# Optimization experiments

Hardware: AMD Instinct MI355X
Metric: run time of the kernel (lower is better)

Reference implementation:

```python
import jax, jax.numpy as jnp
import numpy as np

B, T, D = 4, 2048, 2048
H = 16
HO = D // H  # head_out = 128


def setup_inputs() -> dict:
    key = jax.random.key(0)
    ks = jax.random.split(key, 6)
    x = jax.random.normal(ks[0], (B, T, D), dtype=jnp.float32)
    scale = 0.02
    Wq = jax.random.normal(ks[1], (D, D), dtype=jnp.float32) * scale
    Wk = jax.random.normal(ks[2], (D, D), dtype=jnp.float32) * scale
    Wv = jax.random.normal(ks[3], (D, D), dtype=jnp.float32) * scale
    Wp = jax.random.normal(ks[4], (D, D), dtype=jnp.float32) * scale
    bp = jnp.zeros((D,), dtype=jnp.float32)
    return {"x": x, "Wq": Wq, "Wk": Wk, "Wv": Wv, "Wp": Wp, "bp": bp}


def reference(x, Wq, Wk, Wv, Wp, bp):
    b, t, _ = x.shape
    # QKV projections (weights stored [d_in, d_out])
    q = x @ Wq
    k = x @ Wk
    v = x @ Wv
    split = lambda a: a.reshape(b, t, H, HO).transpose(0, 2, 1, 3)  # [b,H,T,ho]
    qh, kh, vh = split(q), split(k), split(v)
    # Feature attention: contract over tokens -> [b,H,ho,ho]
    scores = jnp.einsum('bhtf,bhtg->bhfg', qh, kh) / jnp.sqrt(jnp.float32(HO))
    weights = jax.nn.softmax(scores, axis=-1)  # dropout p=0.0 (identity)
    # feature_alibi: [1/T, 1/(T-1), ..., 1], broadcast over batch/head/feature
    feat_alibi = (1.0 / jnp.arange(t, 0, -1, dtype=jnp.float32)).reshape(1, 1, t, 1)
    vh = vh + feat_alibi
    # (weights @ v^T)^T : ctx[b,h,t,f] = sum_g weights[b,h,f,g] * v[b,h,t,g]
    ctx = jnp.einsum('bhfg,bhtg->bhtf', weights, vh)
    ctx = ctx.transpose(0, 2, 1, 3).reshape(b, t, H * HO)  # [b,T,d_out]
    return ctx @ Wp + bp
```

## Files before the change

kernel.cpp:

```cpp
#include <hip/hip_runtime.h>
#include <hip/hip_bf16.h>


#define Tt 2048
#define Dd 2048
#define Mm 8192

typedef __attribute__((ext_vector_type(4))) float f32x4;
typedef __attribute__((ext_vector_type(8))) short s16x8;
static_assert(sizeof(s16x8) == 16, "frag size");

typedef const __attribute__((address_space(1))) void* gptr_t;
typedef __attribute__((address_space(3))) void* lptr_t;

__device__ __forceinline__ float bf2f(ushort u) {
    union { unsigned int i; float f; } c; c.i = ((unsigned int)u) << 16; return c.f;
}
__device__ __forceinline__ ushort f2bf(float f) {
    union { float f; unsigned int i; } c; c.f = f;
    return (ushort)((c.i + 0x7FFFu + ((c.i >> 16) & 1u)) >> 16);
}
__device__ __forceinline__ void gload16(const void* g, void* l) {
    __builtin_amdgcn_global_load_lds((gptr_t)g, (lptr_t)l, 16, 0, 0);
}
__device__ __forceinline__ s16x8 ldfrag(const char* p) { return *(const s16x8*)p; }

#define MFMA_BF16(d, a, b) \
    asm("v_mfma_f32_16x16x32_bf16 %0, %1, %2, %0" : "+v"(d) : "v"(a), "v"(b))


__global__ __launch_bounds__(256) void convx_kernel(const float* __restrict__ x,
                                                    ushort* __restrict__ xb) {
    const int idx = blockIdx.x * 256 + threadIdx.x;
    const int stride = gridDim.x * 256;
    for (int i = idx; i < Mm * Dd / 4; i += stride) {
        const float4 v = *(const float4*)(x + (size_t)i * 4);
        ushort4 o; o.x = f2bf(v.x); o.y = f2bf(v.y); o.z = f2bf(v.z); o.w = f2bf(v.w);
        *(ushort4*)(xb + (size_t)i * 4) = o;
    }
}

__global__ __launch_bounds__(256) void transw_kernel(const float* __restrict__ W0,
        const float* __restrict__ W1, const float* __restrict__ W2,
        const float* __restrict__ W3, ushort* __restrict__ Wt) {
    __shared__ float tile[64][65];
    const int z = blockIdx.z;
    const float* W = (z == 0) ? W0 : (z == 1) ? W1 : (z == 2) ? W2 : W3;
    ushort* dst = Wt + (size_t)z * ((size_t)Dd * Dd);
    const int n0 = blockIdx.x * 64, k0 = blockIdx.y * 64;
    const int r4 = threadIdx.x >> 6, c = threadIdx.x & 63;
#pragma unroll
    for (int i = 0; i < 16; i++) {
        const int row = i * 4 + r4;
        tile[row][c] = W[(size_t)(k0 + row) * Dd + n0 + c];
    }
    __syncthreads();
#pragma unroll
    for (int i = 0; i < 16; i++) {
        const int row = i * 4 + r4;
        dst[(size_t)(n0 + row) * Dd + k0 + c] = f2bf(tile[c][row]);
    }
}


__device__ __forceinline__ void stage_half(char* ldsRegion, const ushort* gRegion,
                                           int ld, int half, int tid) {
#pragma unroll
    for (int j = 0; j < 2; j++) {
        const int Pb = half * 16384 + j * 8192 + (tid >> 6) * 1024;
        const int P = Pb + (tid & 63) * 16;
        const int row = P >> 7;
        const int colb = (P ^ ((row & 7) << 4)) & 127;
        gload16(gRegion + (size_t)row * ld + (colb >> 1), ldsRegion + Pb);
    }
}

template <int MODE>
__global__ __launch_bounds__(512, 2) void gemm256_kernel(
        const ushort* __restrict__ A, const ushort* __restrict__ Bt,
        void* __restrict__ Cv, const float* __restrict__ bias,
        int Kdim, int lda, int ldb, int ldc,
        size_t bstride, size_t cstride) {
    extern __shared__ char lds[];

    const int tid = threadIdx.x;
    const int lane = tid & 63;
    const int w = tid >> 6;
    const int wr = w >> 2, wc = w & 3;
    const int fr = lane & 15, fq = lane >> 4;

    const int bid = blockIdx.x;
    const int wg = (bid & 7) * 32 + (bid >> 3);
    const int m0 = (wg >> 3) * 256;
    const int n0 = (wg & 7) * 256;

    const ushort* Ag = A + (size_t)m0 * lda;
    const ushort* Bg = Bt + (size_t)blockIdx.z * bstride + (size_t)n0 * ldb;
    const int NT = Kdim >> 6;

    const int aoff = wr * 16384 + fr * 128;
    const int boff = wc * 8192 + fr * 128;
    const int xo = (fr & 7) << 4;
    const int cp0 = (fq * 16) ^ xo;
    const int cp1 = (64 + fq * 16) ^ xo;

    f32x4 acc[8][4];
#pragma unroll
    for (int i = 0; i < 8; i++)
#pragma unroll
        for (int j = 0; j < 4; j++) acc[i][j] = {0.f, 0.f, 0.f, 0.f};

    s16x8 afX[4][2], afY[4][2], bf01[2][2], bf23[2][2];

    {
        char* b0 = lds;
        char* b1 = lds + 65536;
        stage_half(b0,         Ag, lda, 0, tid);
        stage_half(b0,         Ag, lda, 1, tid);
        stage_half(b0 + 32768, Bg, ldb, 0, tid);
        stage_half(b0 + 32768, Bg, ldb, 1, tid);
        if (NT > 1) {
            stage_half(b1,         Ag + 64, lda, 0, tid);
            stage_half(b1,         Ag + 64, lda, 1, tid);
            stage_half(b1 + 32768, Bg + 64, ldb, 0, tid);
            stage_half(b1 + 32768, Bg + 64, ldb, 1, tid);
        }
        __builtin_amdgcn_sched_barrier(0);
        if (NT > 1) asm volatile("s_waitcnt vmcnt(8)" ::: "memory");
        else        asm volatile("s_waitcnt vmcnt(0)" ::: "memory");
        __builtin_amdgcn_s_barrier();
    }

    for (int t = 0; t < NT; ++t) {
        char* bufc = lds + (t & 1) * 65536;
        const char* Ab = bufc + aoff;
        const char* Bb = bufc + 32768 + boff;
        const ushort* Ag2 = Ag + (size_t)(t + 2) * 64;
        const ushort* Bg2 = Bg + (size_t)(t + 2) * 64;

#pragma unroll
        for (int m = 0; m < 4; m++) {
            afX[m][0] = ldfrag(Ab + m * 2048 + cp0);
            afX[m][1] = ldfrag(Ab + m * 2048 + cp1);
        }
#pragma unroll
        for (int n = 0; n < 2; n++) {
            bf01[n][0] = ldfrag(Bb + n * 2048 + cp0);
            bf01[n][1] = ldfrag(Bb + n * 2048 + cp1);
        }
        __builtin_amdgcn_sched_barrier(0);
        __builtin_amdgcn_s_barrier();
        asm volatile("s_waitcnt lgkmcnt(0)" ::: "memory");
        __builtin_amdgcn_sched_barrier(0);
        __builtin_amdgcn_s_setprio(1);
#pragma unroll
        for (int k = 0; k < 2; k++)
#pragma unroll
            for (int m = 0; m < 4; m++)
#pragma unroll
                for (int n = 0; n < 2; n++) MFMA_BF16(acc[m][n], afX[m][k], bf01[n][k]);
        __builtin_amdgcn_s_setprio(0);
        __builtin_amdgcn_s_barrier();

#pragma unroll
        for (int n = 0; n < 2; n++) {
            bf23[n][0] = ldfrag(Bb + (n + 2) * 2048 + cp0);
            bf23[n][1] = ldfrag(Bb + (n + 2) * 2048 + cp1);
        }
        __builtin_amdgcn_sched_barrier(0);
        __builtin_amdgcn_s_barrier();
        asm volatile("s_waitcnt lgkmcnt(0)" ::: "memory");
        __builtin_amdgcn_sched_barrier(0);
        __builtin_amdgcn_s_setprio(1);
#pragma unroll
        for (int k = 0; k < 2; k++)
#pragma unroll
            for (int m = 0; m < 4; m++)
#pragma unroll
                for (int n = 0; n < 2; n++) MFMA_BF16(acc[m][n + 2], afX[m][k], bf23[n][k]);
        __builtin_amdgcn_s_setprio(0);
        __builtin_amdgcn_s_barrier();

        if (t + 2 < NT) {
            stage_half(bufc + 32768, Bg2, ldb, 0, tid);
            stage_half(bufc + 32768, Bg2, ldb, 1, tid);
        }
#pragma unroll
        for (int m = 0; m < 4; m++) {
            afY[m][0] = ldfrag(Ab + (m + 4) * 2048 + cp0);
            afY[m][1] = ldfrag(Ab + (m + 4) * 2048 + cp1);
        }
        __builtin_amdgcn_sched_barrier(0);
        __builtin_amdgcn_s_barrier();
        asm volatile("s_waitcnt lgkmcnt(0)" ::: "memory");
        __builtin_amdgcn_sched_barrier(0);
        __builtin_amdgcn_s_setprio(1);
#pragma unroll
        for (int k = 0; k < 2; k++)
#pragma unroll
            for (int m = 0; m < 4; m++)
#pragma unroll
                for (int n = 0; n < 2; n++) MFMA_BF16(acc[m + 4][n], afY[m][k], bf01[n][k]);
        __builtin_amdgcn_s_setprio(0);
        __builtin_amdgcn_s_barrier();

        if (t + 2 < NT) {
            stage_half(bufc, Ag2, lda, 0, tid);
            stage_half(bufc, Ag2, lda, 1, tid);
        }
        __builtin_amdgcn_sched_barrier(0);
        __builtin_amdgcn_s_setprio(1);
#pragma unroll
        for (int k = 0; k < 2; k++)
#pragma unroll
            for (int m = 0; m < 4; m++)
#pragma unroll
                for (int n = 0; n < 2; n++) MFMA_BF16(acc[m + 4][n + 2], afY[m][k], bf23[n][k]);
        __builtin_amdgcn_s_setprio(0);
        __builtin_amdgcn_sched_barrier(0);
        if (t + 2 < NT) asm volatile("s_waitcnt vmcnt(8)" ::: "memory");
        else            asm volatile("s_waitcnt vmcnt(0)" ::: "memory");
        __builtin_amdgcn_sched_barrier(0);
        __builtin_amdgcn_s_barrier();
    }

    asm volatile("s_nop 7\ns_nop 7\ns_nop 7");

    if (MODE == 2) {
        float* C = (float*)Cv;
#pragma unroll
        for (int mi = 0; mi < 8; mi++)
#pragma unroll
            for (int ni = 0; ni < 4; ni++)
#pragma unroll
                for (int r = 0; r < 4; r++) {
                    const int row = m0 + wr * 128 + mi * 16 + fq * 4 + r;
                    const int col = n0 + wc * 64 + ni * 16 + fr;
                    C[(size_t)row * ldc + col] = acc[mi][ni][r] + bias[col];
                }
    } else {
        ushort* C = (ushort*)Cv + (size_t)blockIdx.z * cstride;
#pragma unroll
        for (int mi = 0; mi < 8; mi++)
#pragma unroll
            for (int ni = 0; ni < 4; ni++)
#pragma unroll
                for (int r = 0; r < 4; r++) {
                    const int row = m0 + wr * 128 + mi * 16 + fq * 4 + r;
                    const int col = n0 + wc * 64 + ni * 16 + fr;
                    C[(size_t)row * ldc + col] = f2bf(acc[mi][ni][r]);
                }
    }
}


template <int MODE>
__global__ __launch_bounds__(256, 2) void gemm_kernel(
        const ushort* __restrict__ A, const ushort* __restrict__ Bt,
        void* __restrict__ Cv, const float* __restrict__ bias,
        int Kdim, int lda, int ldb, int ldc) {
    __shared__ ushort lsA[128 * 32];
    __shared__ ushort lsB[128 * 32];

    const int tid = threadIdx.x;
    const int w = tid >> 6, lane = tid & 63;
    const int m0 = blockIdx.y * 128;
    const int n0 = blockIdx.x * 128;

    const ushort* Ab = A;
    const ushort* Bb = Bt;
    size_t coff = 0;
    if (MODE == 1) {
        const int z = blockIdx.z, b = z >> 4, h = z & 15;
        const size_t ao = (size_t)b * ((size_t)Tt * Dd) + (size_t)h * 128;
        Ab += ao; Bb += (size_t)z * (128 * 128); coff = ao;
    }

    const int sr = lane >> 2;
    const int sc = (lane & 3) * 8;
    const int c0 = w, c1 = w + 4;
    const int rA0 = c0 * 16 + sr, rA1 = c1 * 16 + sr;

    const int fr = lane & 15, fq = lane >> 4;
    const int wr = (w >> 1) * 64, wc = (w & 1) * 64;

    f32x4 acc[4][4];
#pragma unroll
    for (int i = 0; i < 4; i++)
#pragma unroll
        for (int j = 0; j < 4; j++) acc[i][j] = {0.f, 0.f, 0.f, 0.f};

    for (int kt = 0; kt < Kdim; kt += 32) {
        gload16(Ab + (size_t)(m0 + rA0) * lda + kt + sc, lsA + c0 * 512);
        gload16(Ab + (size_t)(m0 + rA1) * lda + kt + sc, lsA + c1 * 512);
        gload16(Bb + (size_t)(n0 + rA0) * ldb + kt + sc, lsB + c0 * 512);
        gload16(Bb + (size_t)(n0 + rA1) * ldb + kt + sc, lsB + c1 * 512);
        __syncthreads();

        s16x8 afrag[4], bfrag[4];
#pragma unroll
        for (int i = 0; i < 4; i++)
            afrag[i] = *(const s16x8*)(lsA + (wr + i * 16 + fr) * 32 + fq * 8);
#pragma unroll
        for (int j = 0; j < 4; j++)
            bfrag[j] = *(const s16x8*)(lsB + (wc + j * 16 + fr) * 32 + fq * 8);
#pragma unroll
        for (int i = 0; i < 4; i++)
#pragma unroll
            for (int j = 0; j < 4; j++)
                MFMA_BF16(acc[i][j], afrag[i], bfrag[j]);
        __syncthreads();
    }

    asm volatile("s_nop 7\ns_nop 7\ns_nop 7");

    {
        ushort* C = (ushort*)Cv + coff;
#pragma unroll
        for (int i = 0; i < 4; i++)
#pragma unroll
            for (int j = 0; j < 4; j++)
#pragma unroll
                for (int r = 0; r < 4; r++) {
                    const int row = m0 + wr + i * 16 + fq * 4 + r;
                    const int col = n0 + wc + j * 16 + fr;
                    float val = acc[i][j][r];
                    if (MODE == 1) val += 1.0f / (float)(Tt - row);
                    C[(size_t)row * ldc + col] = f2bf(val);
                }
    }
}


__global__ __launch_bounds__(256) void scores_kernel(const ushort* __restrict__ q,
        const ushort* __restrict__ k, float* __restrict__ part) {
    __shared__ float lsQ[32][128];
    __shared__ float lsK[32][128];
    const int tid = threadIdx.x;
    const int s = blockIdx.x, bh = blockIdx.y;
    const int b = bh >> 4, h = bh & 15;
    const size_t base = (size_t)b * ((size_t)Tt * Dd) + (size_t)h * 128;
    const ushort* qb = q + base;
    const ushort* kb = k + base;
    const int ty = tid >> 4, tx = tid & 15;
    const int f0 = ty * 8, g0 = tx * 8;

    float acc[8][8];
#pragma unroll
    for (int i = 0; i < 8; i++)
#pragma unroll
        for (int j = 0; j < 8; j++) acc[i][j] = 0.f;

    for (int ch = 0; ch < 16; ch++) {
        const int t0 = s * 512 + ch * 32;
#pragma unroll
        for (int ii = 0; ii < 4; ii++) {
            const int e = ii * 1024 + tid * 4;
            const int r = e >> 7, cc = e & 127;
            const size_t ga = (size_t)(t0 + r) * Dd + cc;
            const ushort4 v4 = *(const ushort4*)(qb + ga);
            f32x4 qf = {bf2f(v4.x), bf2f(v4.y), bf2f(v4.z), bf2f(v4.w)};
            *(f32x4*)&lsQ[r][cc] = qf;
            const ushort4 w4 = *(const ushort4*)(kb + ga);
            f32x4 kf = {bf2f(w4.x), bf2f(w4.y), bf2f(w4.z), bf2f(w4.w)};
            *(f32x4*)&lsK[r][cc] = kf;
        }
        __syncthreads();
#pragma unroll 4
        for (int tl = 0; tl < 32; tl++) {
            float qv[8], kv[8];
            *(f32x4*)&qv[0] = *(const f32x4*)&lsQ[tl][f0];
            *(f32x4*)&qv[4] = *(const f32x4*)&lsQ[tl][f0 + 4];
            *(f32x4*)&kv[0] = *(const f32x4*)&lsK[tl][g0];
            *(f32x4*)&kv[4] = *(const f32x4*)&lsK[tl][g0 + 4];
#pragma unroll
            for (int i = 0; i < 8; i++)
#pragma unroll
                for (int j = 0; j < 8; j++)
                    acc[i][j] = fmaf(qv[i], kv[j], acc[i][j]);
        }
        __syncthreads();
    }
    float* pb = part + ((size_t)s * 64 + bh) * 16384;
#pragma unroll
    for (int i = 0; i < 8; i++) {
        f32x4 o0 = {acc[i][0], acc[i][1], acc[i][2], acc[i][3]};
        f32x4 o1 = {acc[i][4], acc[i][5], acc[i][6], acc[i][7]};
        *(f32x4*)&pb[(f0 + i) * 128 + g0] = o0;
        *(f32x4*)&pb[(f0 + i) * 128 + g0 + 4] = o1;
    }
}


__global__ __launch_bounds__(256) void softmax_kernel(const float* __restrict__ part,
                                                      ushort* __restrict__ wts) {
    const int tid = threadIdx.x;
    const int wv = tid >> 6, lane = tid & 63;
    const int row = blockIdx.x * 4 + wv;
    const float* p = part + (size_t)row * 128 + lane * 2;
    float v0 = 0.f, v1 = 0.f;
#pragma unroll
    for (int s = 0; s < 4; s++) {
        const float2 t = *(const float2*)(p + (size_t)s * 1048576);
        v0 += t.x; v1 += t.y;
    }
    const float sc = 0.088388347648318447f;
    v0 *= sc; v1 *= sc;
    float m = fmaxf(v0, v1);
#pragma unroll
    for (int off = 32; off > 0; off >>= 1) m = fmaxf(m, __shfl_xor(m, off));
    const float e0 = __expf(v0 - m), e1 = __expf(v1 - m);
    float smv = e0 + e1;
#pragma unroll
    for (int off = 32; off > 0; off >>= 1) smv += __shfl_xor(smv, off);
    const float inv = 1.0f / smv;
    ushort2 o; o.x = f2bf(e0 * inv); o.y = f2bf(e1 * inv);
    *(ushort2*)(wts + (size_t)row * 128 + lane * 2) = o;
}


extern "C" void kernel_launch(void* const* d_in, const int* in_sizes, int n_in,
                              void* d_out, int out_size, void* d_ws, size_t ws_size,
                              hipStream_t stream) {
    const float* x  = (const float*)d_in[0];
    const float* Wq = (const float*)d_in[1];
    const float* Wk = (const float*)d_in[2];
    const float* Wv = (const float*)d_in[3];
    const float* Wp = (const float*)d_in[4];
    const float* bp = (const float*)d_in[5];
    float* out = (float*)d_out;
    char* ws = (char*)d_ws;

    ushort* xb   = (ushort*)(ws);
    ushort* Wt   = (ushort*)(ws + (33ull << 20));
    ushort* q    = (ushort*)(ws + (65ull << 20));
    ushort* k    = (ushort*)(ws + (97ull << 20));
    ushort* v    = (ushort*)(ws + (129ull << 20));
    float*  part = (float*) (ws + (161ull << 20));
    ushort* wts  = (ushort*)(ws + (193ull << 20));
    ushort* ctx  = xb;

    const size_t WSZ = (size_t)Dd * Dd;
    const size_t QSTRIDE = (32ull << 20) / 2;

    static_cast<void>(hipFuncSetAttribute((const void*)gemm256_kernel<0>,
        hipFuncAttributeMaxDynamicSharedMemorySize, 131072));
    static_cast<void>(hipFuncSetAttribute((const void*)gemm256_kernel<2>,
        hipFuncAttributeMaxDynamicSharedMemorySize, 131072));

    convx_kernel<<<2048, 256, 0, stream>>>(x, xb);
    transw_kernel<<<dim3(32, 32, 4), 256, 0, stream>>>(Wq, Wk, Wv, Wp, Wt);

    gemm256_kernel<0><<<dim3(256, 1, 3), 512, 131072, stream>>>(
        xb, Wt, q, nullptr, 2048, 2048, 2048, 2048, WSZ, QSTRIDE);

    scores_kernel<<<dim3(4, 64), 256, 0, stream>>>(q, k, part);
    softmax_kernel<<<2048, 256, 0, stream>>>(part, wts);

    gemm_kernel<1><<<dim3(1, 16, 64), 256, 0, stream>>>(v, wts, ctx, nullptr, 128, 2048, 128, 2048);

    gemm256_kernel<2><<<dim3(256, 1, 1), 512, 131072, stream>>>(
        ctx, Wt + 3 * WSZ, out, bp, 2048, 2048, 2048, 2048, 0, 0);
}
```

Baseline: 379.5 us.

## Unroll GEMM main loop by two and spread global-to-LDS staging across phases

The K loop now runs two tiles per iteration with fixed pointers into both LDS buffers, which removes per-iteration buffer address arithmetic. Global-to-LDS staging is split into half-loads issued in every compute phase instead of bunched in two phases, and the wait counts change to match. The aim is to overlap memory traffic more evenly with MFMA work. The loop now assumes NT is even and at least two, and the hand-tuned vmcnt/lgkmcnt values must stay exactly right or the kernel races.

```diff
diff --git a/kernel.cpp b/kernel.cpp
--- a/kernel.cpp
+++ b/kernel.cpp
@@ -104,6 +104,13 @@
     const int cp0 = (fq * 16) ^ xo;
     const int cp1 = (64 + fq * 16) ^ xo;
 
+    char* buf0 = lds;
+    char* buf1 = lds + 65536;
+    const char* Ab0 = buf0 + aoff;
+    const char* Bb0 = buf0 + 32768 + boff;
+    const char* Ab1 = buf1 + aoff;
+    const char* Bb1 = buf1 + 32768 + boff;
+
     f32x4 acc[8][4];
 #pragma unroll
     for (int i = 0; i < 8; i++)
@@ -113,42 +120,43 @@
     s16x8 afX[4][2], afY[4][2], bf01[2][2], bf23[2][2];
 
     {
-        char* b0 = lds;
-        char* b1 = lds + 65536;
-        stage_half(b0,         Ag, lda, 0, tid);
-        stage_half(b0,         Ag, lda, 1, tid);
-        stage_half(b0 + 32768, Bg, ldb, 0, tid);
-        stage_half(b0 + 32768, Bg, ldb, 1, tid);
-        if (NT > 1) {
-            stage_half(b1,         Ag + 64, lda, 0, tid);
-            stage_half(b1,         Ag + 64, lda, 1, tid);
-            stage_half(b1 + 32768, Bg + 64, ldb, 0, tid);
-            stage_half(b1 + 32768, Bg + 64, ldb, 1, tid);
-        }
-        __builtin_amdgcn_sched_barrier(0);
-        if (NT > 1) asm volatile("s_waitcnt vmcnt(8)" ::: "memory");
-        else        asm volatile("s_waitcnt vmcnt(0)" ::: "memory");
-        __builtin_amdgcn_s_barrier();
-    }
-
-    for (int t = 0; t < NT; ++t) {
-        char* bufc = lds + (t & 1) * 65536;
-        const char* Ab = bufc + aoff;
-        const char* Bb = bufc + 32768 + boff;
-        const ushort* Ag2 = Ag + (size_t)(t + 2) * 64;
-        const ushort* Bg2 = Bg + (size_t)(t + 2) * 64;
+        stage_half(buf0,         Ag, lda, 0, tid);
+        stage_half(buf0,         Ag, lda, 1, tid);
+        stage_half(buf0 + 32768, Bg, ldb, 0, tid);
+        stage_half(buf0 + 32768, Bg, ldb, 1, tid);
+        stage_half(buf1,         Ag + 64, lda, 0, tid);
+        stage_half(buf1,         Ag + 64, lda, 1, tid);
+        stage_half(buf1 + 32768, Bg + 64, ldb, 0, tid);
+        stage_half(buf1 + 32768, Bg + 64, ldb, 1, tid);
+        __builtin_amdgcn_sched_barrier(0);
+        asm volatile("s_waitcnt vmcnt(8)" ::: "memory");
+        __builtin_amdgcn_s_barrier();
+    }
+
+    const int NI = NT >> 1;
+    for (int j = 0; j < NI; ++j) {
+        const int e = 2 * j;
+        const bool sAo = (j > 0);
+        const bool sE2 = (e + 2 < NT);
+        const bool sO2 = (e + 3 < NT);
+        const ushort* AgO  = Ag + (size_t)(e + 1) * 64;
+        const ushort* AgE2 = Ag + (size_t)(e + 2) * 64;
+        const ushort* BgE2 = Bg + (size_t)(e + 2) * 64;
+        const ushort* BgO2 = Bg + (size_t)(e + 3) * 64;
 
 #pragma unroll
         for (int m = 0; m < 4; m++) {
-            afX[m][0] = ldfrag(Ab + m * 2048 + cp0);
-            afX[m][1] = ldfrag(Ab + m * 2048 + cp1);
+            afX[m][0] = ldfrag(Ab0 + m * 2048 + cp0);
+            afX[m][1] = ldfrag(Ab0 + m * 2048 + cp1);
         }
 #pragma unroll
         for (int n = 0; n < 2; n++) {
-            bf01[n][0] = ldfrag(Bb + n * 2048 + cp0);
-            bf01[n][1] = ldfrag(Bb + n * 2048 + cp1);
-        }
-        __builtin_amdgcn_sched_barrier(0);
+            bf01[n][0] = ldfrag(Bb0 + n * 2048 + cp0);
+            bf01[n][1] = ldfrag(Bb0 + n * 2048 + cp1);
+        }
+        if (sAo) stage_half(buf1, AgO, lda, 0, tid);
+        __builtin_amdgcn_sched_barrier(0);
+        asm volatile("s_waitcnt lgkmcnt(8)" ::: "memory");
         __builtin_amdgcn_s_barrier();
         asm volatile("s_waitcnt lgkmcnt(0)" ::: "memory");
         __builtin_amdgcn_sched_barrier(0);
@@ -164,9 +172,10 @@
 
 #pragma unroll
         for (int n = 0; n < 2; n++) {
-            bf23[n][0] = ldfrag(Bb + (n + 2) * 2048 + cp0);
-            bf23[n][1] = ldfrag(Bb + (n + 2) * 2048 + cp1);
-        }
+            bf23[n][0] = ldfrag(Bb0 + (n + 2) * 2048 + cp0);
+            bf23[n][1] = ldfrag(Bb0 + (n + 2) * 2048 + cp1);
+        }
+        if (sAo) stage_half(buf1, AgO, lda, 1, tid);
         __builtin_amdgcn_sched_barrier(0);
         __builtin_amdgcn_s_barrier();
         asm volatile("s_waitcnt lgkmcnt(0)" ::: "memory");
@@ -181,15 +190,12 @@
         __builtin_amdgcn_s_setprio(0);
         __builtin_amdgcn_s_barrier();
 
-        if (t + 2 < NT) {
-            stage_half(bufc + 32768, Bg2, ldb, 0, tid);
-            stage_half(bufc + 32768, Bg2, ldb, 1, tid);
-        }
 #pragma unroll
         for (int m = 0; m < 4; m++) {
-            afY[m][0] = ldfrag(Ab + (m + 4) * 2048 + cp0);
-            afY[m][1] = ldfrag(Ab + (m + 4) * 2048 + cp1);
-        }
+            afY[m][0] = ldfrag(Ab0 + (m + 4) * 2048 + cp0);
+            afY[m][1] = ldfrag(Ab0 + (m + 4) * 2048 + cp1);
+        }
+        if (sE2) stage_half(buf0 + 32768, BgE2, ldb, 0, tid);
         __builtin_amdgcn_sched_barrier(0);
         __builtin_amdgcn_s_barrier();
         asm volatile("s_waitcnt lgkmcnt(0)" ::: "memory");
@@ -204,10 +210,7 @@
         __builtin_amdgcn_s_setprio(0);
         __builtin_amdgcn_s_barrier();
 
-        if (t + 2 < NT) {
-            stage_half(bufc, Ag2, lda, 0, tid);
-            stage_half(bufc, Ag2, lda, 1, tid);
-        }
+        if (sE2) stage_half(buf0 + 32768, BgE2, ldb, 1, tid);
         __builtin_amdgcn_sched_barrier(0);
         __builtin_amdgcn_s_setprio(1);
 #pragma unroll
@@ -218,9 +221,89 @@
                 for (int n = 0; n < 2; n++) MFMA_BF16(acc[m + 4][n + 2], afY[m][k], bf23[n][k]);
         __builtin_amdgcn_s_setprio(0);
         __builtin_amdgcn_sched_barrier(0);
-        if (t + 2 < NT) asm volatile("s_waitcnt vmcnt(8)" ::: "memory");
-        else            asm volatile("s_waitcnt vmcnt(0)" ::: "memory");
-        __builtin_amdgcn_sched_barrier(0);
+        if (sE2) asm volatile("s_waitcnt vmcnt(4)" ::: "memory");
+        else     asm volatile("s_waitcnt vmcnt(0)" ::: "memory");
+        __builtin_amdgcn_s_barrier();
+
+#pragma unroll
+        for (int m = 0; m < 4; m++) {
+            afX[m][0] = ldfrag(Ab1 + m * 2048 + cp0);
+            afX[m][1] = ldfrag(Ab1 + m * 2048 + cp1);
+        }
+#pragma unroll
+        for (int n = 0; n < 2; n++) {
+            bf01[n][0] = ldfrag(Bb1 + n * 2048 + cp0);
+            bf01[n][1] = ldfrag(Bb1 + n * 2048 + cp1);
+        }
+        if (sE2) stage_half(buf0, AgE2, lda, 0, tid);
+        __builtin_amdgcn_sched_barrier(0);
+        asm volatile("s_waitcnt lgkmcnt(8)" ::: "memory");
+        __builtin_amdgcn_s_barrier();
+        asm volatile("s_waitcnt lgkmcnt(0)" ::: "memory");
+        __builtin_amdgcn_sched_barrier(0);
+        __builtin_amdgcn_s_setprio(1);
+#pragma unroll
+        for (int k = 0; k < 2; k++)
+#pragma unroll
+            for (int m = 0; m < 4; m++)
+#pragma unroll
+                for (int n = 0; n < 2; n++) MFMA_BF16(acc[m][n], afX[m][k], bf01[n][k]);
+        __builtin_amdgcn_s_setprio(0);
+        __builtin_amdgcn_s_barrier();
+
+#pragma unroll
+        for (int n = 0; n < 2; n++) {
+            bf23[n][0] = ldfrag(Bb1 + (n + 2) * 2048 + cp0);
+            bf23[n][1] = ldfrag(Bb1 + (n + 2) * 2048 + cp1);
+        }
+        if (sE2) stage_half(buf0, AgE2, lda, 1, tid);
+        __builtin_amdgcn_sched_barrier(0);
+        __builtin_amdgcn_s_barrier();
+        asm volatile("s_waitcnt lgkmcnt(0)" ::: "memory");
+        __builtin_amdgcn_sched_barrier(0);
+        __builtin_amdgcn_s_setprio(1);
+#pragma unroll
+        for (int k = 0; k < 2; k++)
+#pragma unroll
+            for (int m = 0; m < 4; m++)
+#pragma unroll
+                for (int n = 0; n < 2; n++) MFMA_BF16(acc[m][n + 2], afX[m][k], bf23[n][k]);
+        __builtin_amdgcn_s_setprio(0);
+        __builtin_amdgcn_s_barrier();
+
+#pragma unroll
+        for (int m = 0; m < 4; m++) {
+            afY[m][0] = ldfrag(Ab1 + (m + 4) * 2048 + cp0);
+            afY[m][1] = ldfrag(Ab1 + (m + 4) * 2048 + cp1);
+        }
+        if (sO2) stage_half(buf1 + 32768, BgO2, ldb, 0, tid);
+        __builtin_amdgcn_sched_barrier(0);
+        __builtin_amdgcn_s_barrier();
+        asm volatile("s_waitcnt lgkmcnt(0)" ::: "memory");
+        __builtin_amdgcn_sched_barrier(0);
+        __builtin_amdgcn_s_setprio(1);
+#pragma unroll
+        for (int k = 0; k < 2; k++)
+#pragma unroll
+            for (int m = 0; m < 4; m++)
+#pragma unroll
+                for (int n = 0; n < 2; n++) MFMA_BF16(acc[m + 4][n], afY[m][k], bf01[n][k]);
+        __builtin_amdgcn_s_setprio(0);
+        __builtin_amdgcn_s_barrier();
+
+        if (sO2) stage_half(buf1 + 32768, BgO2, ldb, 1, tid);
+        __builtin_amdgcn_sched_barrier(0);
+        __builtin_amdgcn_s_setprio(1);
+#pragma unroll
+        for (int k = 0; k < 2; k++)
+#pragma unroll
+            for (int m = 0; m < 4; m++)
+#pragma unroll
+                for (int n = 0; n < 2; n++) MFMA_BF16(acc[m + 4][n + 2], afY[m][k], bf23[n][k]);
+        __builtin_amdgcn_s_setprio(0);
+        __builtin_amdgcn_sched_barrier(0);
+        if (sO2) asm volatile("s_waitcnt vmcnt(4)" ::: "memory");
+        else     asm volatile("s_waitcnt vmcnt(0)" ::: "memory");
         __builtin_amdgcn_s_barrier();
     }
 
```

Result: no change. 376.8 us (-0.7%).
